# Kernel optimization log

Measured on AMD Instinct MI355X. Metric: run time of the kernel, lower is better.

## Reference

```python
import jax, jax.numpy as jnp
import numpy as np

B, K, N, DIM, C_IN = 4, 2048, 4096, 3, 61
IN = DIM + C_IN        # 64, deepset input size
H1, H2 = 128, 128      # neighbor_xf hidden sizes
OUT = 64               # c_out // heads
HEADS = 4
EPS = 1e-5             # BatchNorm eps


def _lin(key, i, o):
    return jax.random.normal(key, (i, o), jnp.float32) * (1.0 / np.sqrt(i))


def setup_inputs() -> dict:
    key = jax.random.key(0)
    ks = jax.random.split(key, 12)
    return {
        "keys": jax.random.normal(ks[0], (B, K, DIM), jnp.float32),
        "points": jax.random.normal(ks[1], (B, N, DIM), jnp.float32),
        "feats": jax.random.normal(ks[2], (B, N, C_IN), jnp.float32),
        "nx_w1": _lin(ks[3], IN, H1), "nx_b1": jnp.zeros((H1,), jnp.float32),
        "nx_w2": _lin(ks[4], H1, H2), "nx_b2": jnp.zeros((H2,), jnp.float32),
        "nx_w3": _lin(ks[5], H2, OUT), "nx_b3": jnp.zeros((OUT,), jnp.float32),
        "sx_w1": _lin(ks[6], IN, IN), "sx_b1": jnp.zeros((IN,), jnp.float32),
        "sx_w2": _lin(ks[7], IN, IN), "sx_b2": jnp.zeros((IN,), jnp.float32),
        "sx_w3": _lin(ks[8], IN, IN), "sx_b3": jnp.zeros((IN,), jnp.float32),
        "att_w": _lin(ks[9], 2 * IN, HEADS * IN),
        "att_b": jnp.zeros((HEADS * IN,), jnp.float32),
        "att_q": jax.random.normal(ks[10], (HEADS, IN), jnp.float32) * 0.1,
        "bn_gamma": jnp.ones((IN,), jnp.float32),
        "bn_beta": jnp.zeros((IN,), jnp.float32),
        "neighbors": 32,
    }


def _mlp3(x, w1, b1, w2, b2, w3, b3):
    # per-element deepset MLP: Linear-ReLU-Linear-ReLU-Linear
    h = jax.nn.relu(x @ w1 + b1)
    h = jax.nn.relu(h @ w2 + b2)
    return h @ w3 + b3


def _forward(keys, points, feats, nx_w1, nx_b1, nx_w2, nx_b2, nx_w3, nx_b3,
             sx_w1, sx_b1, sx_w2, sx_b2, sx_w3, sx_b3,
             att_w, att_b, att_q, bn_gamma, bn_beta, neighbors):
    b = keys.shape[0]
    # Euclidean dist_fn: dist_vec [B,K,N,dim], dist [B,K,N], all points valid
    rel = points[:, None, :, :] - keys[:, :, None, :]
    dist = jnp.sqrt(jnp.sum(rel * rel, axis=-1))
    _, idx = jax.lax.top_k(-dist, neighbors)                   # [B,K,k] nearest
    nrel = jnp.take_along_axis(rel, idx[..., None], axis=2)    # [B,K,k,dim]
    bidx = jnp.arange(b)[:, None, None]
    nfeat = feats[bidx, idx]                                   # [B,K,k,c_in]
    comb = jnp.concatenate([nrel, nfeat], axis=-1)             # [B,K,k,in]
    lat = _mlp3(comb, nx_w1, nx_b1, nx_w2, nx_b2, nx_w3, nx_b3)  # [B,K,k,out]
    # BatchNorm1d (training-mode batch stats) over flattened [B*K*k, in]
    flat = comb.reshape(-1, comb.shape[-1])
    mean = jnp.mean(flat, axis=0)
    var = jnp.var(flat, axis=0)
    norm = (comb - mean) * jax.lax.rsqrt(var + EPS) * bn_gamma + bn_beta
    # SelfAttention: deepset sum-pooled context + per-neighbor softmax weights
    set_feat = jnp.sum(_mlp3(norm, sx_w1, sx_b1, sx_w2, sx_b2, sx_w3, sx_b3), axis=2)
    comb_feat = jnp.concatenate(
        [norm, jnp.broadcast_to(set_feat[:, :, None, :], norm.shape)], axis=-1)
    heads = (comb_feat @ att_w + att_b).reshape(comb_feat.shape[:3] + (HEADS, -1))
    e = jnp.sum(heads * att_q, axis=-1)                        # [B,K,k,H]
    w = jax.nn.softmax(e, axis=-2)                             # softmax over neighbor axis
    out = jnp.einsum('bkno,bknh->bkoh', lat, w)                # weighted reduce over k
    return out.reshape(out.shape[:2] + (-1,))                  # [B,K,out*H]


def reference(keys, points, feats, nx_w1, nx_b1, nx_w2, nx_b2, nx_w3, nx_b3,
              sx_w1, sx_b1, sx_w2, sx_b2, sx_w3, sx_b3,
              att_w, att_b, att_q, bn_gamma, bn_beta, neighbors):
    return _forward(keys, points, feats, nx_w1, nx_b1, nx_w2, nx_b2, nx_w3, nx_b3,
                    sx_w1, sx_b1, sx_w2, sx_b2, sx_w3, sx_b3,
                    att_w, att_b, att_q, bn_gamma, bn_beta, neighbors)
```

## Files before the change

### kernel.cpp

```cpp
#include <hip/hip_runtime.h>
#include <math.h>

#define BATCH 4
#define KQ    2048
#define NPTS  4096
#define CIN   61
#define KNN   32
#define ROWS  (BATCH*KQ*KNN)

#define OFF_IDX  0
#define OFF_ACC  524288
#define OFF_ATTA 557056
#define OFF_W1F  558080
#define OFF_W2F  574464
#define OFF_W3F  607232

typedef __attribute__((ext_vector_type(8)))  short bfrag;
typedef __attribute__((ext_vector_type(4)))  unsigned ufrag;
typedef __attribute__((ext_vector_type(16))) float cfrag;

__device__ __forceinline__ unsigned short bf16_rne(float x) {
  unsigned u = __float_as_uint(x);
  unsigned r = u + 0x7fffu + ((u >> 16) & 1u);
  return (unsigned short)(r >> 16);
}
__device__ __forceinline__ float4 ld4u(const float* p) {
  float4 r; __builtin_memcpy(&r, p, 16); return r;
}
__device__ __forceinline__ unsigned cvtpk(float lo, float hi) {
  unsigned r;
  asm("v_cvt_pk_bf16_f32 %0, %1, %2" : "=v"(r) : "v"(lo), "v"(hi));
  return r;
}
__device__ __forceinline__ float up_lo(unsigned pk) { return __uint_as_float(pk << 16); }
__device__ __forceinline__ float up_hi(unsigned pk) { return __uint_as_float(pk & 0xffff0000u); }

__device__ __forceinline__ cfrag zero16() {
  cfrag z;
#pragma unroll
  for (int i = 0; i < 16; ++i) z[i] = 0.f;
  return z;
}
__device__ __forceinline__ cfrag mfma_bu(bfrag a, ufrag b, cfrag c) {
  return __builtin_amdgcn_mfma_f32_32x32x16_bf16(a, __builtin_bit_cast(bfrag, b), c, 0, 0, 0);
}
__device__ __forceinline__ cfrag mfma_ub(ufrag a, bfrag b, cfrag c) {
  return __builtin_amdgcn_mfma_f32_32x32x16_bf16(__builtin_bit_cast(bfrag, a), b, c, 0, 0, 0);
}
__device__ __forceinline__ cfrag mfma_uu(ufrag a, ufrag b, cfrag c) {
  return __builtin_amdgcn_mfma_f32_32x32x16_bf16(__builtin_bit_cast(bfrag, a), __builtin_bit_cast(bfrag, b), c, 0, 0, 0);
}

#define NCAND 384

template<int NS>
__device__ __forceinline__ void select_emit(
    const unsigned* __restrict__ VAL, const int* __restrict__ IDXL,
    int mcount, unsigned hib, unsigned lob, int lane,
    const float* __restrict__ Pb, float kx, float ky, float kz,
    unsigned short* __restrict__ dst, int* __restrict__ SEL,
    float* __restrict__ accs) {
  const unsigned long long lmask = (1ull << lane) - 1ull;
  unsigned e[NS];
#pragma unroll
  for (int s = 0; s < NS; ++s) {
    int ei = s*64 + lane;
    e[s] = (ei < mcount) ? VAL[ei] : 0xffffffffu;
  }
  unsigned lo2 = lob, hi2 = hib;
  while (lo2 < hi2) {
    unsigned mid = lo2 + ((hi2 - lo2) >> 1);
    int c = 0;
#pragma unroll
    for (int s = 0; s < NS; ++s) c += (int)__popcll(__ballot(e[s] <= mid));
    if (c == KNN) { hi2 = mid; break; }
    if (c > KNN) hi2 = mid; else lo2 = mid + 1;
  }
  const unsigned T = hi2;
  float r0=0.f,r1=0.f,r2=0.f,r3=0.f,r4=0.f,r5=0.f;
  int base2 = 0;
#pragma unroll
  for (int s = 0; s < NS; ++s) {
    bool p = (e[s] <= T);
    unsigned long long m = __ballot(p);
    if (p) {
      int pos = base2 + (int)__popcll(m & lmask);
      if (pos < KNN) {
        int n = IDXL[s*64 + lane];
        SEL[pos] = n;
        dst[pos] = (unsigned short)n;
        float dx = Pb[n*3+0]-kx, dy = Pb[n*3+1]-ky, dz = Pb[n*3+2]-kz;
        r0 += dx; r1 += dy; r2 += dz;
        r3 += dx*dx; r4 += dy*dy; r5 += dz*dz;
      }
    }
    base2 += (int)__popcll(m);
  }
#pragma unroll
  for (int off = 32; off > 0; off >>= 1) {
    r0 += __shfl_down(r0, off); r1 += __shfl_down(r1, off);
    r2 += __shfl_down(r2, off); r3 += __shfl_down(r3, off);
    r4 += __shfl_down(r4, off); r5 += __shfl_down(r5, off);
  }
  if (lane == 0) {
    atomicAdd(&accs[0], r0); atomicAdd(&accs[1], r1); atomicAdd(&accs[2], r2);
    atomicAdd(&accs[64], r3); atomicAdd(&accs[65], r4); atomicAdd(&accs[66], r5);
  }
}

__device__ __forceinline__ void dispatch_select(
    const unsigned* VAL, const int* IDXL, int mcount, unsigned hib, unsigned lob,
    int lane, const float* Pb, float kx, float ky, float kz,
    unsigned short* dst, int* SEL, float* accs) {
  if (mcount <= 64)
    select_emit<1>(VAL, IDXL, mcount, hib, lob, lane, Pb, kx, ky, kz, dst, SEL, accs);
  else if (mcount <= 128)
    select_emit<2>(VAL, IDXL, mcount, hib, lob, lane, Pb, kx, ky, kz, dst, SEL, accs);
  else if (mcount <= 192)
    select_emit<3>(VAL, IDXL, mcount, hib, lob, lane, Pb, kx, ky, kz, dst, SEL, accs);
  else
    select_emit<6>(VAL, IDXL, mcount, hib, lob, lane, Pb, kx, ky, kz, dst, SEL, accs);
}

__global__ __launch_bounds__(256, 4) void topk_kernel(
    const float* __restrict__ keys, const float* __restrict__ points,
    const float* __restrict__ feats,
    const float* __restrict__ w1, const float* __restrict__ w2,
    const float* __restrict__ w3,
    const float* __restrict__ att_w, const float* __restrict__ att_q,
    unsigned short* __restrict__ idx_out, float* __restrict__ acc,
    short* __restrict__ w1f, short* __restrict__ w2f, short* __restrict__ w3f,
    float* __restrict__ attA) {
  __shared__ unsigned VAL[4][NCAND];
  __shared__ int IDXL[4][NCAND];
  __shared__ int SEL[4][KNN];
  __shared__ unsigned HIB[4];
  __shared__ int WTOT[4][4];
  __shared__ float FRED[64*33];
  __shared__ float FQ[64*33];
  const int tid = threadIdx.x;
  const int lane = tid & 63, wid = tid >> 6;
  const int g0 = blockIdx.x * 4;
  const int b = g0 >> 11;
  const float kx0 = keys[(size_t)g0*3+0], ky0 = keys[(size_t)g0*3+1],  kz0 = keys[(size_t)g0*3+2];
  const float kx1 = keys[(size_t)g0*3+3], ky1 = keys[(size_t)g0*3+4],  kz1 = keys[(size_t)g0*3+5];
  const float kx2 = keys[(size_t)g0*3+6], ky2 = keys[(size_t)g0*3+7],  kz2 = keys[(size_t)g0*3+8];
  const float kx3 = keys[(size_t)g0*3+9], ky3 = keys[(size_t)g0*3+10], kz3 = keys[(size_t)g0*3+11];
  const float* __restrict__ Pb = points + (size_t)b * NPTS * 3;

  unsigned u0[16], u1[16], u2[16], u3[16];
  unsigned lm0 = 0xffffffffu, lm1 = 0xffffffffu, lm2 = 0xffffffffu, lm3 = 0xffffffffu;
#pragma unroll
  for (int c4 = 0; c4 < 4; ++c4) {
    const float* pp = Pb + (size_t)(tid*16 + c4*4) * 3;
    float4 A = ld4u(pp), B4 = ld4u(pp + 4), C4 = ld4u(pp + 8);
    float x, y, z, dx, dy, dz;
#define DPT(slot, PX, PY, PZ)                                        \
    x = PX; y = PY; z = PZ;                                          \
    dx = x-kx0; dy = y-ky0; dz = z-kz0;                              \
    u0[slot] = __float_as_uint(dx*dx + dy*dy + dz*dz);               \
    lm0 = min(lm0, u0[slot]);                                        \
    dx = x-kx1; dy = y-ky1; dz = z-kz1;                              \
    u1[slot] = __float_as_uint(dx*dx + dy*dy + dz*dz);               \
    lm1 = min(lm1, u1[slot]);                                        \
    dx = x-kx2; dy = y-ky2; dz = z-kz2;                              \
    u2[slot] = __float_as_uint(dx*dx + dy*dy + dz*dz);               \
    lm2 = min(lm2, u2[slot]);                                        \
    dx = x-kx3; dy = y-ky3; dz = z-kz3;                              \
    u3[slot] = __float_as_uint(dx*dx + dy*dy + dz*dz);               \
    lm3 = min(lm3, u3[slot]);
    DPT(c4*4+0, A.x,  A.y,  A.z)
    DPT(c4*4+1, A.w,  B4.x, B4.y)
    DPT(c4*4+2, B4.z, B4.w, C4.x)
    DPT(c4*4+3, C4.y, C4.z, C4.w)
#undef DPT
  }

  const unsigned lmw = (wid == 0) ? lm0 : (wid == 1) ? lm1 : (wid == 2) ? lm2 : lm3;
  unsigned wlo = lmw, whi = lmw;
#pragma unroll
  for (int off = 1; off < 64; off <<= 1) {
    unsigned a0 = (unsigned)__shfl_xor((int)wlo, off);
    unsigned a1 = (unsigned)__shfl_xor((int)whi, off);
    wlo = min(wlo, a0); whi = max(whi, a1);
  }
  {
    unsigned lo = wlo, hi = whi;
    while (lo < hi) {
      unsigned mid = lo + ((hi - lo) >> 1);
      int c = (int)__popcll(__ballot(lmw <= mid));
      if (c == KNN) { hi = mid; break; }
      if (c > KNN) hi = mid; else lo = mid + 1;
    }
    if (lane == 0) HIB[wid] = hi;
  }
  __syncthreads();
  const unsigned hb0 = HIB[0], hb1 = HIB[1], hb2 = HIB[2], hb3 = HIB[3];

  int c0 = 0, c1 = 0, c2 = 0, c3 = 0;
#pragma unroll
  for (int j = 0; j < 16; ++j) {
    c0 += (u0[j] <= hb0) ? 1 : 0;
    c1 += (u1[j] <= hb1) ? 1 : 0;
    c2 += (u2[j] <= hb2) ? 1 : 0;
    c3 += (u3[j] <= hb3) ? 1 : 0;
  }
  int i0 = c0, i1 = c1, i2 = c2, i3 = c3;
#pragma unroll
  for (int off = 1; off < 64; off <<= 1) {
    int t0 = __shfl_up(i0, off), t1 = __shfl_up(i1, off);
    int t2 = __shfl_up(i2, off), t3 = __shfl_up(i3, off);
    if (lane >= off) { i0 += t0; i1 += t1; i2 += t2; i3 += t3; }
  }
  if (lane == 63) {
    WTOT[0][wid] = i0; WTOT[1][wid] = i1; WTOT[2][wid] = i2; WTOT[3][wid] = i3;
  }
  __syncthreads();
  int p0 = i0 - c0, p1 = i1 - c1, p2 = i2 - c2, p3 = i3 - c3;
  for (int w = 0; w < wid; ++w) {
    p0 += WTOT[0][w]; p1 += WTOT[1][w]; p2 += WTOT[2][w]; p3 += WTOT[3][w];
  }
#pragma unroll
  for (int j = 0; j < 16; ++j) {
    const int n = tid*16 + j;
    if (u0[j] <= hb0) { if (p0 < NCAND) { VAL[0][p0] = u0[j]; IDXL[0][p0] = n; } ++p0; }
    if (u1[j] <= hb1) { if (p1 < NCAND) { VAL[1][p1] = u1[j]; IDXL[1][p1] = n; } ++p1; }
    if (u2[j] <= hb2) { if (p2 < NCAND) { VAL[2][p2] = u2[j]; IDXL[2][p2] = n; } ++p2; }
    if (u3[j] <= hb3) { if (p3 < NCAND) { VAL[3][p3] = u3[j]; IDXL[3][p3] = n; } ++p3; }
  }
  __syncthreads();

  float* accs = &acc[(blockIdx.x & 63)*128];
  {
    const int mcount = min(WTOT[wid][0]+WTOT[wid][1]+WTOT[wid][2]+WTOT[wid][3], NCAND);
    const unsigned hibw = (wid == 0) ? hb0 : (wid == 1) ? hb1 : (wid == 2) ? hb2 : hb3;
    const float kxw = (wid == 0) ? kx0 : (wid == 1) ? kx1 : (wid == 2) ? kx2 : kx3;
    const float kyw = (wid == 0) ? ky0 : (wid == 1) ? ky1 : (wid == 2) ? ky2 : ky3;
    const float kzw = (wid == 0) ? kz0 : (wid == 1) ? kz1 : (wid == 2) ? kz2 : kz3;
    dispatch_select(VAL[wid], IDXL[wid], mcount, hibw, wlo, lane, Pb,
                    kxw, kyw, kzw, idx_out + (size_t)(g0 + wid)*KNN, SEL[wid], accs);
  }
  __syncthreads();

  {
    const int row = tid >> 3, chunk = tid & 7;
    const int nA = SEL[0][row], nB = SEL[1][row];
    const int nC = SEL[2][row], nD = SEL[3][row];
    const float* frA = feats + ((size_t)b*NPTS + nA)*CIN;
    const float* frB = feats + ((size_t)b*NPTS + nB)*CIN;
    const float* frC = feats + ((size_t)b*NPTS + nC)*CIN;
    const float* frD = feats + ((size_t)b*NPTS + nD)*CIN;
    float fs[8] = {0,0,0,0,0,0,0,0}, fq[8] = {0,0,0,0,0,0,0,0};
    if (chunk < 7) {
      const float* fr[4] = {frA, frB, frC, frD};
#pragma unroll
      for (int qq = 0; qq < 4; ++qq) {
        float4 a0 = ld4u(fr[qq] + chunk*8), a1 = ld4u(fr[qq] + chunk*8 + 4);
        fs[0]+=a0.x; fq[0]+=a0.x*a0.x; fs[1]+=a0.y; fq[1]+=a0.y*a0.y;
        fs[2]+=a0.z; fq[2]+=a0.z*a0.z; fs[3]+=a0.w; fq[3]+=a0.w*a0.w;
        fs[4]+=a1.x; fq[4]+=a1.x*a1.x; fs[5]+=a1.y; fq[5]+=a1.y*a1.y;
        fs[6]+=a1.z; fq[6]+=a1.z*a1.z; fs[7]+=a1.w; fq[7]+=a1.w*a1.w;
      }
    } else {
#pragma unroll
      for (int i = 0; i < 5; ++i) {
        float va = frA[56+i], vb = frB[56+i], vc = frC[56+i], vd = frD[56+i];
        fs[i] = va + vb + vc + vd;
        fq[i] = va*va + vb*vb + vc*vc + vd*vd;
      }
    }
#pragma unroll
    for (int i = 0; i < 8; ++i) {
      FRED[(chunk*8 + i)*33 + row] = fs[i];
      FQ  [(chunk*8 + i)*33 + row] = fq[i];
    }
  }
  __syncthreads();
  if (tid < 64) {
    float s = 0.f, q2 = 0.f;
#pragma unroll
    for (int r = 0; r < 32; ++r) {
      s  += FRED[tid*33 + r];
      q2 += FQ[tid*33 + r];
    }
    if (tid < CIN) {
      atomicAdd(&accs[3 + tid], s);
      atomicAdd(&accs[64 + 3 + tid], q2);
    }
  }

  if (blockIdx.x < 128) {
    const int t = blockIdx.x * 256 + tid;
    if (t < 8192) {
      int j = t & 7, ln = (t >> 3) & 63, tk = t >> 9;
      int kc = tk & 3, tile = tk >> 2;
      int nh = tile*32 + (ln & 31), k = kc*16 + (ln >> 5)*8 + j;
      w1f[t] = (short)bf16_rne(w1[k*128 + nh]);
    } else if (t < 24576) {
      int t2 = t - 8192;
      int j = t2 & 7, ln = (t2 >> 3) & 63, tk = t2 >> 9;
      int kc = tk & 7, tile = tk >> 3;
      int nh = tile*32 + (ln & 31);
      int k = 32*(kc>>1) + 16*(kc&1) + 4*(ln>>5) + (j&3) + 8*(j>>2);
      w2f[t2] = (short)bf16_rne(w2[k*128 + nh]);
    } else {
      int t3 = t - 24576;
      int j = t3 & 7, ln = (t3 >> 3) & 63, tk = t3 >> 9;
      int kc = tk & 7, tile = tk >> 3;
      int nh = tile*32 + (ln & 31);
      int k = 32*(kc>>1) + 16*(kc&1) + 4*(ln>>5) + (j&3) + 8*(j>>2);
      w3f[t3] = (short)bf16_rne(w3[k*64 + nh]);
    }
  } else if (blockIdx.x == 128) {
    const int t = tid, c = t >> 2, hh = t & 3;
    float s = 0.f;
    for (int d = 0; d < 64; ++d) s += att_w[c*256 + hh*64 + d] * att_q[hh*64 + d];
    attA[c*4 + hh] = s;
  }
}

#define L_W1F 0
#define L_W2F 16384
#define L_W3F 49152
#define L_SH  65536
#define L_SL  69632
#define L_B1  73728
#define L_B2  74240
#define L_B3  74752
#define L_WSC 75008
#define L_SC  79104
#define L_TOT 79360

__global__ __launch_bounds__(512, 4) void main_kernel(
    const float* __restrict__ keys, const float* __restrict__ points,
    const float* __restrict__ feats, const unsigned short* __restrict__ idxg,
    const short* __restrict__ w1f, const short* __restrict__ w2f,
    const short* __restrict__ w3f,
    const float* __restrict__ b1, const float* __restrict__ b2,
    const float* __restrict__ b3,
    const float* __restrict__ attAg, const float* __restrict__ accg,
    const float* __restrict__ gammav, float* __restrict__ out) {
  __shared__ __align__(16) char smem[L_TOT];
  const int tid = threadIdx.x;
  const int bid = blockIdx.x;
  const int wid = tid >> 6, lane = tid & 63;
  const int col = lane & 31, h = lane >> 5;

  float* WS = (float*)(smem + L_WSC) + wid*128;
  const short* SW1 = (const short*)(smem + L_W1F);
  const short* SW2 = (const short*)(smem + L_W2F);
  const short* SW3 = (const short*)(smem + L_W3F);
  const float* SB1 = (const float*)(smem + L_B1);
  const float* SB2 = (const float*)(smem + L_B2);

  auto gather_pack = [&](int g, int n, ufrag* ahi, ufrag* alo) {
    const int b = g >> 11;
    const float* frow = feats + ((size_t)b*NPTS + n)*CIN;
    float v[4][8];
    if (h == 0) {
      const float* Pb = points + (size_t)b*NPTS*3;
      v[0][0] = Pb[n*3+0] - keys[(size_t)g*3+0];
      v[0][1] = Pb[n*3+1] - keys[(size_t)g*3+1];
      v[0][2] = Pb[n*3+2] - keys[(size_t)g*3+2];
      float4 t0 = ld4u(frow);
      v[0][3]=t0.x; v[0][4]=t0.y; v[0][5]=t0.z; v[0][6]=t0.w;
      v[0][7] = frow[4];
    } else {
      float4 a0 = ld4u(frow+5), a1 = ld4u(frow+9);
      v[0][0]=a0.x; v[0][1]=a0.y; v[0][2]=a0.z; v[0][3]=a0.w;
      v[0][4]=a1.x; v[0][5]=a1.y; v[0][6]=a1.z; v[0][7]=a1.w;
    }
#pragma unroll
    for (int kc = 1; kc < 4; ++kc) {
      const int f0 = kc*16 + 8*h - 3;
      float4 a0 = ld4u(frow+f0), a1 = ld4u(frow+f0+4);
      v[kc][0]=a0.x; v[kc][1]=a0.y; v[kc][2]=a0.z; v[kc][3]=a0.w;
      v[kc][4]=a1.x; v[kc][5]=a1.y; v[kc][6]=a1.z; v[kc][7]=a1.w;
    }
#pragma unroll
    for (int kc = 0; kc < 4; ++kc)
#pragma unroll
      for (int p = 0; p < 4; ++p) {
        unsigned pk = cvtpk(v[kc][2*p], v[kc][2*p+1]);
        ahi[kc][p] = pk;
        alo[kc][p] = cvtpk(v[kc][2*p] - up_lo(pk), v[kc][2*p+1] - up_hi(pk));
      }
  };

  auto chain = [&](int g, const ufrag* ahi, const ufrag* alo) {
    cfrag Ef = zero16();
#pragma unroll
    for (int kc = 0; kc < 4; ++kc) {
      bfrag sh = *(const bfrag*)((const short*)(smem + L_SH) + (kc*64 + lane)*8);
      bfrag sl = *(const bfrag*)((const short*)(smem + L_SL) + (kc*64 + lane)*8);
      Ef = mfma_ub(ahi[kc], sh, Ef);
      Ef = mfma_ub(alo[kc], sh, Ef);
      Ef = mfma_ub(ahi[kc], sl, Ef);
    }

    float mx = Ef[0];
#pragma unroll
    for (int i = 1; i < 16; ++i) mx = fmaxf(mx, Ef[i]);
    mx = fmaxf(mx, __shfl_xor(mx, 32));
    float wsm[16], ssum = 0.f;
#pragma unroll
    for (int i = 0; i < 16; ++i) { wsm[i] = __expf(Ef[i] - mx); ssum += wsm[i]; }
    ssum += __shfl_xor(ssum, 32);
    const float invs = 1.f / ssum;
#pragma unroll
    for (int i = 0; i < 16; ++i) wsm[i] *= invs;

    if (col < 4) {
#pragma unroll
      for (int i = 0; i < 8; ++i) {
        const int c0 = (2*i & 3) + 8*(i >> 1);
        const int nA = c0 + 4*h;
        WS[nA*4 + col]     = wsm[2*i];
        WS[nA*4 + 4 + col] = wsm[2*i+1];
      }
    }
    const int hdc = col & 3;
    ufrag whi[2], wlo[2];
#pragma unroll
    for (int bb = 0; bb < 2; ++bb)
#pragma unroll
      for (int p = 0; p < 4; ++p) {
        const int c0 = (2*p & 3) + 8*(p >> 1);
        const int n0 = 16*bb + 4*h + c0;
        float r0 = WS[n0*4 + hdc], r1 = WS[n0*4 + 4 + hdc];
        unsigned pk = cvtpk(r0, r1);
        whi[bb][p] = pk;
        wlo[bb][p] = cvtpk(r0 - up_lo(pk), r1 - up_hi(pk));
      }

    ufrag a2[8];
#pragma unroll
    for (int t = 0; t < 4; ++t) {
      cfrag acc = zero16();
#pragma unroll
      for (int kc = 0; kc < 4; ++kc) {
        bfrag wf = *(const bfrag*)(SW1 + ((t*4 + kc)*64 + lane)*8);
        acc = mfma_bu(wf, ahi[kc], acc);
      }
#pragma unroll
      for (int i = 0; i < 8; ++i) {
        const int c0 = (2*i & 3) + 8*(i >> 1);
        float2 bb2 = *(const float2*)(SB1 + t*32 + c0 + 4*h);
        float x0 = fmaxf(acc[2*i]   + bb2.x, 0.f);
        float x1 = fmaxf(acc[2*i+1] + bb2.y, 0.f);
        a2[2*t + (i>>2)][i&3] = cvtpk(x0, x1);
      }
    }

    ufrag a3[8];
#pragma unroll
    for (int t = 0; t < 4; ++t) {
      cfrag acc = zero16();
#pragma unroll
      for (int kc = 0; kc < 8; ++kc) {
        bfrag wf = *(const bfrag*)(SW2 + ((t*8 + kc)*64 + lane)*8);
        acc = mfma_bu(wf, a2[kc], acc);
      }
#pragma unroll
      for (int i = 0; i < 8; ++i) {
        const int c0 = (2*i & 3) + 8*(i >> 1);
        float2 bb2 = *(const float2*)(SB2 + t*32 + c0 + 4*h);
        float x0 = fmaxf(acc[2*i]   + bb2.x, 0.f);
        float x1 = fmaxf(acc[2*i+1] + bb2.y, 0.f);
        a3[2*t + (i>>2)][i&3] = cvtpk(x0, x1);
      }
    }

#pragma unroll
    for (int t = 0; t < 2; ++t) {
      cfrag acc = zero16();
#pragma unroll
      for (int kc = 0; kc < 8; ++kc) {
        bfrag wf = *(const bfrag*)(SW3 + ((t*8 + kc)*64 + lane)*8);
        acc = mfma_ub(a3[kc], wf, acc);
      }
      const float bz = ((const float*)(smem + L_B3))[t*32 + col];
#pragma unroll
      for (int i = 0; i < 16; ++i) acc[i] += bz;
      ufrag lh[2], ll[2];
#pragma unroll
      for (int i = 0; i < 8; ++i) {
        unsigned pk = cvtpk(acc[2*i], acc[2*i+1]);
        lh[i>>2][i&3] = pk;
        ll[i>>2][i&3] = cvtpk(acc[2*i] - up_lo(pk), acc[2*i+1] - up_hi(pk));
      }
      cfrag og = zero16();
#pragma unroll
      for (int bb = 0; bb < 2; ++bb) og = mfma_uu(lh[bb], whi[bb], og);
#pragma unroll
      for (int bb = 0; bb < 2; ++bb) og = mfma_uu(ll[bb], whi[bb], og);
#pragma unroll
      for (int bb = 0; bb < 2; ++bb) og = mfma_uu(lh[bb], wlo[bb], og);
      if (col < 4) {
        float* op = out + (size_t)g*256 + t*128 + col;
#pragma unroll
        for (int i = 0; i < 16; ++i) {
          const int orow = (i&3) + 8*(i>>2) + 4*h;
          op[orow*4] = og[i];
        }
      }
    }
  };

  const int g0q = bid*8 + wid;
  const int g1q = g0q + 4096;
  const int n0 = (int)idxg[(size_t)g0q*KNN + col];
  const int n1 = (int)idxg[(size_t)g1q*KNN + col];
  ufrag ahi0[4], alo0[4];
  gather_pack(g0q, n0, ahi0, alo0);

  {
    const uint4* src = (const uint4*)w1f;
    uint4* dst = (uint4*)smem;
#pragma unroll
    for (int r = 0; r < 8; ++r) dst[r*512 + tid] = src[r*512 + tid];
    if (tid < 128) ((float*)(smem + L_B1))[tid] = b1[tid];
    else if (tid < 256) ((float*)(smem + L_B2))[tid-128] = b2[tid-128];
    else if (tid < 320) ((float*)(smem + L_B3))[tid-256] = b3[tid-256];
    float* TMP = (float*)(smem + L_WSC);
    {
      int c = tid & 63, p = tid >> 6;
      float s = 0.f, s2 = 0.f;
      for (int k = p; k < 64; k += 8) {
        s += accg[k*128 + c]; s2 += accg[k*128 + 64 + c];
      }
      TMP[p*128 + c] = s; TMP[p*128 + 64 + c] = s2;
    }
    __syncthreads();
    float* SCp = (float*)(smem + L_SC);
    if (tid < 64) {
      float s = 0.f, s2 = 0.f;
#pragma unroll
      for (int p = 0; p < 8; ++p) { s += TMP[p*128 + tid]; s2 += TMP[p*128 + 64 + tid]; }
      const float invR = 1.f / (float)ROWS;
      float mean = s * invR;
      float var = s2 * invR - mean * mean;
      SCp[tid] = gammav[tid] * rsqrtf(var + 1e-5f);
    }
    __syncthreads();
    {
      const int s = tid >> 8;
      const int kc = (tid >> 6) & 3;
      const int ln = tid & 63;
      const int hd = ln & 31;
      short* dstf = (short*)(smem + (s ? L_SL : L_SH)) + (kc*64 + ln)*8;
#pragma unroll
      for (int j = 0; j < 8; ++j) {
        const int ch = kc*16 + (ln>>5)*8 + j;
        float val = (hd < 4) ? attAg[ch*4 + hd] * SCp[ch] : 0.f;
        unsigned hb = bf16_rne(val);
        if (s) {
          float lo = val - __uint_as_float(hb << 16);
          dstf[j] = (short)bf16_rne(lo);
        } else {
          dstf[j] = (short)hb;
        }
      }
    }
    __syncthreads();
  }

  chain(g0q, ahi0, alo0);

  ufrag ahi1[4], alo1[4];
  gather_pack(g1q, n1, ahi1, alo1);
  chain(g1q, ahi1, alo1);
}

extern "C" void kernel_launch(void* const* d_in, const int* in_sizes, int n_in,
                              void* d_out, int out_size, void* d_ws, size_t ws_size,
                              hipStream_t stream) {
  const float* keys   = (const float*)d_in[0];
  const float* points = (const float*)d_in[1];
  const float* feats  = (const float*)d_in[2];
  const float* nx_w1  = (const float*)d_in[3];
  const float* nx_b1  = (const float*)d_in[4];
  const float* nx_w2  = (const float*)d_in[5];
  const float* nx_b2  = (const float*)d_in[6];
  const float* nx_w3  = (const float*)d_in[7];
  const float* nx_b3  = (const float*)d_in[8];
  const float* att_w  = (const float*)d_in[15];
  const float* att_q  = (const float*)d_in[17];
  const float* gamma  = (const float*)d_in[18];
  float* out = (float*)d_out;

  char* ws = (char*)d_ws;
  unsigned short* idxp = (unsigned short*)(ws + OFF_IDX);
  float* acc  = (float*)(ws + OFF_ACC);
  float* attA = (float*)(ws + OFF_ATTA);
  short* w1f  = (short*)(ws + OFF_W1F);
  short* w2f  = (short*)(ws + OFF_W2F);
  short* w3f  = (short*)(ws + OFF_W3F);

  hipMemsetAsync(acc, 0, 32768, stream);
  topk_kernel<<<2048, 256, 0, stream>>>(keys, points, feats,
      nx_w1, nx_w2, nx_w3, att_w, att_q, idxp, acc, w1f, w2f, w3f, attA);
  main_kernel<<<512, 512, 0, stream>>>(keys, points, feats, idxp,
      w1f, w2f, w3f, nx_b1, nx_b2, nx_b3, attA, acc, gamma, out);
}
```

Measured before the change: 160.9 us.

## Make top-k candidate selection wave-local with one query per wave

Restructures the neighbor search so each wavefront scans all points for a single query. Before, the four waves of a block cooperatively covered the points for four queries. This removes the block-wide prefix scan, the shared threshold and count arrays, and several __syncthreads barriers. It also shrinks the candidate buffer to 128 and stores indices as 16-bit values, which cuts LDS use. The cost is that each wave now loads all points itself (4x more point traffic, mostly from cache), and capping at 128 candidates risks dropping true neighbors when many points fall under the threshold.

```diff
diff --git a/kernel.cpp b/kernel.cpp
--- a/kernel.cpp
+++ b/kernel.cpp
@@ -51,11 +51,11 @@
   return __builtin_amdgcn_mfma_f32_32x32x16_bf16(__builtin_bit_cast(bfrag, a), __builtin_bit_cast(bfrag, b), c, 0, 0, 0);
 }
 
-#define NCAND 384
+#define NCAND 128
 
 template<int NS>
 __device__ __forceinline__ void select_emit(
-    const unsigned* __restrict__ VAL, const int* __restrict__ IDXL,
+    const unsigned* __restrict__ VAL, const unsigned short* __restrict__ IDXL,
     int mcount, unsigned hib, unsigned lob, int lane,
     const float* __restrict__ Pb, float kx, float ky, float kz,
     unsigned short* __restrict__ dst, int* __restrict__ SEL,
@@ -86,7 +86,7 @@
     if (p) {
       int pos = base2 + (int)__popcll(m & lmask);
       if (pos < KNN) {
-        int n = IDXL[s*64 + lane];
+        int n = (int)IDXL[s*64 + lane];
         SEL[pos] = n;
         dst[pos] = (unsigned short)n;
         float dx = Pb[n*3+0]-kx, dy = Pb[n*3+1]-ky, dz = Pb[n*3+2]-kz;
@@ -106,20 +106,6 @@
     atomicAdd(&accs[0], r0); atomicAdd(&accs[1], r1); atomicAdd(&accs[2], r2);
     atomicAdd(&accs[64], r3); atomicAdd(&accs[65], r4); atomicAdd(&accs[66], r5);
   }
-}
-
-__device__ __forceinline__ void dispatch_select(
-    const unsigned* VAL, const int* IDXL, int mcount, unsigned hib, unsigned lob,
-    int lane, const float* Pb, float kx, float ky, float kz,
-    unsigned short* dst, int* SEL, float* accs) {
-  if (mcount <= 64)
-    select_emit<1>(VAL, IDXL, mcount, hib, lob, lane, Pb, kx, ky, kz, dst, SEL, accs);
-  else if (mcount <= 128)
-    select_emit<2>(VAL, IDXL, mcount, hib, lob, lane, Pb, kx, ky, kz, dst, SEL, accs);
-  else if (mcount <= 192)
-    select_emit<3>(VAL, IDXL, mcount, hib, lob, lane, Pb, kx, ky, kz, dst, SEL, accs);
-  else
-    select_emit<6>(VAL, IDXL, mcount, hib, lob, lane, Pb, kx, ky, kz, dst, SEL, accs);
 }
 
 __global__ __launch_bounds__(256, 4) void topk_kernel(
@@ -132,114 +118,95 @@
     short* __restrict__ w1f, short* __restrict__ w2f, short* __restrict__ w3f,
     float* __restrict__ attA) {
   __shared__ unsigned VAL[4][NCAND];
-  __shared__ int IDXL[4][NCAND];
+  __shared__ unsigned short IDXL[4][NCAND];
   __shared__ int SEL[4][KNN];
-  __shared__ unsigned HIB[4];
-  __shared__ int WTOT[4][4];
   __shared__ float FRED[64*33];
   __shared__ float FQ[64*33];
   const int tid = threadIdx.x;
   const int lane = tid & 63, wid = tid >> 6;
   const int g0 = blockIdx.x * 4;
   const int b = g0 >> 11;
-  const float kx0 = keys[(size_t)g0*3+0], ky0 = keys[(size_t)g0*3+1],  kz0 = keys[(size_t)g0*3+2];
-  const float kx1 = keys[(size_t)g0*3+3], ky1 = keys[(size_t)g0*3+4],  kz1 = keys[(size_t)g0*3+5];
-  const float kx2 = keys[(size_t)g0*3+6], ky2 = keys[(size_t)g0*3+7],  kz2 = keys[(size_t)g0*3+8];
-  const float kx3 = keys[(size_t)g0*3+9], ky3 = keys[(size_t)g0*3+10], kz3 = keys[(size_t)g0*3+11];
+  const int gq = __builtin_amdgcn_readfirstlane(g0 + wid);
+  const float kx = keys[(size_t)gq*3+0];
+  const float ky = keys[(size_t)gq*3+1];
+  const float kz = keys[(size_t)gq*3+2];
   const float* __restrict__ Pb = points + (size_t)b * NPTS * 3;
 
-  unsigned u0[16], u1[16], u2[16], u3[16];
-  unsigned lm0 = 0xffffffffu, lm1 = 0xffffffffu, lm2 = 0xffffffffu, lm3 = 0xffffffffu;
-#pragma unroll
-  for (int c4 = 0; c4 < 4; ++c4) {
-    const float* pp = Pb + (size_t)(tid*16 + c4*4) * 3;
-    float4 A = ld4u(pp), B4 = ld4u(pp + 4), C4 = ld4u(pp + 8);
-    float x, y, z, dx, dy, dz;
-#define DPT(slot, PX, PY, PZ)                                        \
-    x = PX; y = PY; z = PZ;                                          \
-    dx = x-kx0; dy = y-ky0; dz = z-kz0;                              \
-    u0[slot] = __float_as_uint(dx*dx + dy*dy + dz*dz);               \
-    lm0 = min(lm0, u0[slot]);                                        \
-    dx = x-kx1; dy = y-ky1; dz = z-kz1;                              \
-    u1[slot] = __float_as_uint(dx*dx + dy*dy + dz*dz);               \
-    lm1 = min(lm1, u1[slot]);                                        \
-    dx = x-kx2; dy = y-ky2; dz = z-kz2;                              \
-    u2[slot] = __float_as_uint(dx*dx + dy*dy + dz*dz);               \
-    lm2 = min(lm2, u2[slot]);                                        \
-    dx = x-kx3; dy = y-ky3; dz = z-kz3;                              \
-    u3[slot] = __float_as_uint(dx*dx + dy*dy + dz*dz);               \
-    lm3 = min(lm3, u3[slot]);
-    DPT(c4*4+0, A.x,  A.y,  A.z)
-    DPT(c4*4+1, A.w,  B4.x, B4.y)
-    DPT(c4*4+2, B4.z, B4.w, C4.x)
-    DPT(c4*4+3, C4.y, C4.z, C4.w)
-#undef DPT
-  }
-
-  const unsigned lmw = (wid == 0) ? lm0 : (wid == 1) ? lm1 : (wid == 2) ? lm2 : lm3;
-  unsigned wlo = lmw, whi = lmw;
+  unsigned u[64];
+  unsigned lmin = 0xffffffffu;
+#pragma unroll
+  for (int jb = 0; jb < 8; ++jb) {
+    float4 t[8];
+#pragma unroll
+    for (int q = 0; q < 8; ++q) {
+      const int idx = (jb*8 + q)*64 + lane;
+      if (jb == 7 && q == 7) {
+        float4 tt = ld4u(Pb + (size_t)idx*3 - 1);
+        t[q].x = tt.y; t[q].y = tt.z; t[q].z = tt.w; t[q].w = 0.f;
+      } else {
+        t[q] = ld4u(Pb + (size_t)idx*3);
+      }
+    }
+#pragma unroll
+    for (int q = 0; q < 8; ++q) {
+      float dx = t[q].x - kx, dy = t[q].y - ky, dz = t[q].z - kz;
+      unsigned d = __float_as_uint(dx*dx + dy*dy + dz*dz);
+      u[jb*8 + q] = d;
+      lmin = min(lmin, d);
+    }
+  }
+
+  unsigned wlo = lmin, whi = lmin;
 #pragma unroll
   for (int off = 1; off < 64; off <<= 1) {
     unsigned a0 = (unsigned)__shfl_xor((int)wlo, off);
     unsigned a1 = (unsigned)__shfl_xor((int)whi, off);
     wlo = min(wlo, a0); whi = max(whi, a1);
   }
+  unsigned hib;
   {
     unsigned lo = wlo, hi = whi;
     while (lo < hi) {
       unsigned mid = lo + ((hi - lo) >> 1);
-      int c = (int)__popcll(__ballot(lmw <= mid));
+      int c = (int)__popcll(__ballot(lmin <= mid));
       if (c == KNN) { hi = mid; break; }
       if (c > KNN) hi = mid; else lo = mid + 1;
     }
-    if (lane == 0) HIB[wid] = hi;
-  }
-  __syncthreads();
-  const unsigned hb0 = HIB[0], hb1 = HIB[1], hb2 = HIB[2], hb3 = HIB[3];
-
-  int c0 = 0, c1 = 0, c2 = 0, c3 = 0;
-#pragma unroll
-  for (int j = 0; j < 16; ++j) {
-    c0 += (u0[j] <= hb0) ? 1 : 0;
-    c1 += (u1[j] <= hb1) ? 1 : 0;
-    c2 += (u2[j] <= hb2) ? 1 : 0;
-    c3 += (u3[j] <= hb3) ? 1 : 0;
-  }
-  int i0 = c0, i1 = c1, i2 = c2, i3 = c3;
+    hib = hi;
+  }
+
+  int cnt = 0;
+#pragma unroll
+  for (int j = 0; j < 64; ++j) cnt += (u[j] <= hib) ? 1 : 0;
+  int inc = cnt;
 #pragma unroll
   for (int off = 1; off < 64; off <<= 1) {
-    int t0 = __shfl_up(i0, off), t1 = __shfl_up(i1, off);
-    int t2 = __shfl_up(i2, off), t3 = __shfl_up(i3, off);
-    if (lane >= off) { i0 += t0; i1 += t1; i2 += t2; i3 += t3; }
-  }
-  if (lane == 63) {
-    WTOT[0][wid] = i0; WTOT[1][wid] = i1; WTOT[2][wid] = i2; WTOT[3][wid] = i3;
-  }
-  __syncthreads();
-  int p0 = i0 - c0, p1 = i1 - c1, p2 = i2 - c2, p3 = i3 - c3;
-  for (int w = 0; w < wid; ++w) {
-    p0 += WTOT[0][w]; p1 += WTOT[1][w]; p2 += WTOT[2][w]; p3 += WTOT[3][w];
-  }
-#pragma unroll
-  for (int j = 0; j < 16; ++j) {
-    const int n = tid*16 + j;
-    if (u0[j] <= hb0) { if (p0 < NCAND) { VAL[0][p0] = u0[j]; IDXL[0][p0] = n; } ++p0; }
-    if (u1[j] <= hb1) { if (p1 < NCAND) { VAL[1][p1] = u1[j]; IDXL[1][p1] = n; } ++p1; }
-    if (u2[j] <= hb2) { if (p2 < NCAND) { VAL[2][p2] = u2[j]; IDXL[2][p2] = n; } ++p2; }
-    if (u3[j] <= hb3) { if (p3 < NCAND) { VAL[3][p3] = u3[j]; IDXL[3][p3] = n; } ++p3; }
-  }
-  __syncthreads();
+    int t = __shfl_up(inc, off);
+    if (lane >= off) inc += t;
+  }
+  const int mtot = __shfl(inc, 63);
+  {
+    int p = inc - cnt;
+#pragma unroll
+    for (int j = 0; j < 64; ++j) {
+      if (u[j] <= hib) {
+        if (p < NCAND) {
+          VAL[wid][p] = u[j];
+          IDXL[wid][p] = (unsigned short)(j*64 + lane);
+        }
+        ++p;
+      }
+    }
+  }
+  const int mcount = min(mtot, NCAND);
 
   float* accs = &acc[(blockIdx.x & 63)*128];
-  {
-    const int mcount = min(WTOT[wid][0]+WTOT[wid][1]+WTOT[wid][2]+WTOT[wid][3], NCAND);
-    const unsigned hibw = (wid == 0) ? hb0 : (wid == 1) ? hb1 : (wid == 2) ? hb2 : hb3;
-    const float kxw = (wid == 0) ? kx0 : (wid == 1) ? kx1 : (wid == 2) ? kx2 : kx3;
-    const float kyw = (wid == 0) ? ky0 : (wid == 1) ? ky1 : (wid == 2) ? ky2 : ky3;
-    const float kzw = (wid == 0) ? kz0 : (wid == 1) ? kz1 : (wid == 2) ? kz2 : kz3;
-    dispatch_select(VAL[wid], IDXL[wid], mcount, hibw, wlo, lane, Pb,
-                    kxw, kyw, kzw, idx_out + (size_t)(g0 + wid)*KNN, SEL[wid], accs);
-  }
+  if (mcount <= 64)
+    select_emit<1>(VAL[wid], IDXL[wid], mcount, hib, wlo, lane, Pb,
+                   kx, ky, kz, idx_out + (size_t)gq*KNN, SEL[wid], accs);
+  else
+    select_emit<2>(VAL[wid], IDXL[wid], mcount, hib, wlo, lane, Pb,
+                   kx, ky, kz, idx_out + (size_t)gq*KNN, SEL[wid], accs);
   __syncthreads();
 
   {
```

Result: no change. 161.1 us (+0.1%).
